# Kernel tuning notes

Hardware: AMD Instinct MI355X
Metric: run time of the kernel (lower is better)

The kernel has to match this reference:

```python
import jax, jax.numpy as jnp
import numpy as np
import math

N_HEAD = 16
HEAD_DIM = 64
N_EMBD = N_HEAD * HEAD_DIM  # 1024


def _alibi_slopes(n_heads):
    def pow2(n):
        start = 2.0 ** (-2.0 ** (-(math.log2(n) - 3)))
        return [start * (start ** i) for i in range(n)]
    if n_heads & (n_heads - 1) == 0:
        s = pow2(n_heads)
    else:
        cp2 = 2 ** math.floor(math.log2(n_heads))
        s = pow2(cp2)
        extra_base = 2.0 ** (-2.0 ** (-(math.log2(2 * cp2) - 3)))
        s += [extra_base * (extra_base ** i) for i in range(n_heads - cp2)]
        s = s[:n_heads]
    return jnp.asarray(np.array(s, dtype=np.float32))


def setup_inputs() -> dict:
    key = jax.random.key(0)
    k1, k2, k3, k4 = jax.random.split(key, 4)
    B, T = 2, 2048
    x = jax.random.normal(k1, (B, T, N_EMBD), dtype=jnp.float32)
    # c_attn weight for q,k (use_v=True -> 2*n_embd outputs), no bias
    W_attn = jax.random.normal(k2, (N_EMBD, 2 * N_EMBD), dtype=jnp.float32) * 0.02
    v_tmp = jax.random.normal(k3, (N_HEAD, N_HEAD), dtype=jnp.float32) * 0.02
    proj_tmp = jax.random.normal(k4, (N_HEAD, N_HEAD), dtype=jnp.float32) * 0.02
    return {"x": x, "W_attn": W_attn, "v_tmp": v_tmp, "proj_tmp": proj_tmp}


def reference(x, W_attn, v_tmp, proj_tmp):
    B, T, C = x.shape
    H, D = N_HEAD, HEAD_DIM
    scale = 1.0 / math.sqrt(D)

    qk = x @ W_attn  # (B,T,2C)
    q, k = qk[..., :C], qk[..., C:]
    q = q.reshape(B, T, H, D).transpose(0, 2, 1, 3)  # (B,H,T,D)
    k = k.reshape(B, T, H, D).transpose(0, 2, 1, 3)

    # V via Kronecker-lifted matrix: x @ kron(v_tmp, I_D)
    # block structure => mix head channels: out[...,j,d] = sum_i x[...,i,d]*v_tmp[i,j]
    xh = x.reshape(B, T, H, D)
    v = jnp.einsum('btid,ij->btjd', xh, v_tmp)  # (B,T,H,D)

    scores = jnp.einsum('bhqd,bhkd->bhqk', q, k) * scale  # (B,H,T,T)

    # ALiBi bias + causal mask
    pos = jnp.arange(T, dtype=jnp.float32)
    rel = pos[None, :] - pos[:, None]  # (T,T), mem - ctx
    slopes = _alibi_slopes(H)
    bias = slopes[:, None, None] * rel[None, :, :]
    causal = pos[None, :] <= pos[:, None]
    bias = jnp.where(causal[None, :, :], bias, -jnp.inf)
    scores = scores + bias[None]

    att = jax.nn.softmax(scores, axis=-1)
    y = jnp.einsum('bhqk,bkhd->bqhd', att, v)  # (B,T,H,D)

    # output proj via kron(proj_tmp, I_D).T: out[...,i,d] = sum_j y[...,j,d]*proj_tmp[i,j]
    y = jnp.einsum('btjd,ij->btid', y, proj_tmp)
    return y.reshape(B, T, C)
```

## Files before the change

kernel.cpp:

```cpp
#include <hip/hip_runtime.h>

typedef __attribute__((ext_vector_type(8))) __bf16 bf16x8;
typedef __attribute__((ext_vector_type(8))) unsigned short u16x8;
typedef __attribute__((ext_vector_type(4))) float f32x4;

#define LOG2E 1.4426950408889634f

__device__ __forceinline__ unsigned short f2b(float f) {
  unsigned u = __float_as_uint(f);
  u += 0x7fffu + ((u >> 16) & 1u);
  return (unsigned short)(u >> 16);
}
__device__ __forceinline__ float b2f(unsigned short h) {
  return __uint_as_float(((unsigned)h) << 16);
}

__global__ __launch_bounds__(256) void k_cvt_x(const float* __restrict__ in,
                                               unsigned short* __restrict__ out, int n4) {
  int i = blockIdx.x * blockDim.x + threadIdx.x;
  if (i >= n4) return;
  float4 f = ((const float4*)in)[i];
  ushort4 o;
  o.x = f2b(f.x); o.y = f2b(f.y); o.z = f2b(f.z); o.w = f2b(f.w);
  ((ushort4*)out)[i] = o;
}

__global__ __launch_bounds__(256) void k_trans_w(const float* __restrict__ W,
                                                 unsigned short* __restrict__ Wt) {
  __shared__ unsigned short tile[64][65];
  int n0 = blockIdx.x * 64;
  int k0 = blockIdx.y * 64;
  int tx = threadIdx.x & 63, ty = threadIdx.x >> 6;
#pragma unroll
  for (int r = 0; r < 16; ++r) {
    int kk = ty * 16 + r;
    tile[kk][tx] = f2b(W[(size_t)(k0 + kk) * 2048 + n0 + tx]);
  }
  __syncthreads();
#pragma unroll
  for (int r = 0; r < 16; ++r) {
    int nn = ty * 16 + r;
    Wt[(size_t)(n0 + nn) * 1024 + k0 + tx] = tile[tx][nn];
  }
}

__global__ __launch_bounds__(256) void k_gemm_qk(const unsigned short* __restrict__ A,
                                                 const unsigned short* __restrict__ Bt,
                                                 unsigned short* __restrict__ C) {
  __shared__ unsigned short As[128 * 32];
  __shared__ unsigned short Bs[128 * 32];
  const int K = 1024;
  int m0 = blockIdx.x * 128;
  int n0 = blockIdx.y * 128;
  int tid = threadIdx.x;
  int w = tid >> 6, lane = tid & 63;
  int lq = lane & 15, lk8 = (lane >> 4) * 8;
  int wr = (w >> 1) * 64, wc = (w & 1) * 64;
  f32x4 acc[4][4];
#pragma unroll
  for (int i = 0; i < 4; ++i)
#pragma unroll
    for (int j = 0; j < 4; ++j)
#pragma unroll
      for (int r = 0; r < 4; ++r) acc[i][j][r] = 0.f;

  for (int kk = 0; kk < K; kk += 32) {
    bf16x8 sa[2], sb[2];
#pragma unroll
    for (int i = 0; i < 2; ++i) {
      int c = tid + 256 * i;
      int row = c >> 2, col = (c & 3) * 8;
      sa[i] = *(const bf16x8*)(A + (size_t)(m0 + row) * K + kk + col);
      sb[i] = *(const bf16x8*)(Bt + (size_t)(n0 + row) * K + kk + col);
    }
    __syncthreads();
#pragma unroll
    for (int i = 0; i < 2; ++i) {
      int c = tid + 256 * i;
      int row = c >> 2, col = (c & 3) * 8;
      *(bf16x8*)(As + row * 32 + col) = sa[i];
      *(bf16x8*)(Bs + row * 32 + col) = sb[i];
    }
    __syncthreads();
    bf16x8 af[4], bf[4];
#pragma unroll
    for (int i = 0; i < 4; ++i) af[i] = *(const bf16x8*)(As + (wr + i * 16 + lq) * 32 + lk8);
#pragma unroll
    for (int j = 0; j < 4; ++j) bf[j] = *(const bf16x8*)(Bs + (wc + j * 16 + lq) * 32 + lk8);
#pragma unroll
    for (int i = 0; i < 4; ++i)
#pragma unroll
      for (int j = 0; j < 4; ++j)
        acc[i][j] = __builtin_amdgcn_mfma_f32_16x16x32_bf16(af[i], bf[j], acc[i][j], 0, 0, 0);
  }
#pragma unroll
  for (int i = 0; i < 4; ++i)
#pragma unroll
    for (int j = 0; j < 4; ++j)
#pragma unroll
      for (int r = 0; r < 4; ++r) {
        int m = m0 + wr + i * 16 + (lane >> 4) * 4 + r;
        int n = n0 + wc + j * 16 + lq;
        C[(size_t)m * 2048 + n] = f2b(acc[i][j][r]);
      }
}

__global__ __launch_bounds__(256) void k_vcomp(const float* __restrict__ x,
                                               const float* __restrict__ vt,
                                               unsigned short* __restrict__ vb) {
  __shared__ float s_vt[256];
  s_vt[threadIdx.x] = vt[threadIdx.x];
  __syncthreads();
  int g = blockIdx.x * 256 + threadIdx.x;
  int bt = g >> 6, d = g & 63;
  const float* xp = x + (size_t)bt * 1024 + d;
  float xi[16];
#pragma unroll
  for (int i = 0; i < 16; ++i) xi[i] = xp[i * 64];
#pragma unroll
  for (int j = 0; j < 16; ++j) {
    float s = 0.f;
#pragma unroll
    for (int i = 0; i < 16; ++i) s += xi[i] * s_vt[i * 16 + j];
    vb[(size_t)bt * 1024 + j * 64 + d] = f2b(s);
  }
}

__global__ __launch_bounds__(256) void k_vtrans(const unsigned short* __restrict__ vb,
                                                unsigned short* __restrict__ Vt) {
  __shared__ unsigned short tile[64][65];
  int t0 = blockIdx.x * 64;
  int c0 = blockIdx.y * 64;
  int b = blockIdx.z;
  int tx = threadIdx.x & 63, ty = threadIdx.x >> 6;
#pragma unroll
  for (int r = 0; r < 16; ++r) {
    int tt = ty * 16 + r;
    tile[tt][tx] = vb[((size_t)b * 2048 + t0 + tt) * 1024 + c0 + tx];
  }
  __syncthreads();
#pragma unroll
  for (int r = 0; r < 16; ++r) {
    int cc = ty * 16 + r;
    Vt[((size_t)b * 1024 + c0 + cc) * 2048 + t0 + tx] = tile[tx][cc];
  }
}

__global__ __launch_bounds__(256) void k_flash(const unsigned short* __restrict__ qkb,
                                               const unsigned short* __restrict__ Vt,
                                               unsigned short* __restrict__ y) {
  __shared__ unsigned short Ks[2][2][64 * 32];
  __shared__ unsigned short Vs[2][2][64 * 32];
  __shared__ unsigned short Pbuf[4][16 * 64];
  int hd = blockIdx.y, b = blockIdx.z;
  int tid = threadIdx.x;
  int w = tid >> 6, lane = tid & 63;
  int quad = lane >> 4, lq = lane & 15, lk8 = quad * 8;
  int rs = tid >> 2, cs = (tid & 3) * 8;
  const size_t rowb = (size_t)b * 2048;
  const size_t vrow = ((size_t)b * 1024 + hd * 64 + rs) * 2048 + cs;
  const size_t krow = ((rowb + rs) << 11) + 1024 + hd * 64 + cs;

  float slope = exp2f(-0.5f * (float)(hd + 1));
  const float c1 = 0.125f * LOG2E;
  const float c2 = slope * LOG2E;
  const float SHIFT = 16.0f;

  bf16x8 ones;
#pragma unroll
  for (int i = 0; i < 8; ++i) ones[i] = (__bf16)1.0f;

#pragma unroll 1
  for (int pass = 0; pass < 2; ++pass) {
    int qt = pass ? (31 - (int)blockIdx.x) : (int)blockIdx.x;
    int q0 = qt * 64;
    int qg = q0 + w * 16 + lq;

    bf16x8 qf0 = *(const bf16x8*)(qkb + ((rowb + qg) << 11) + hd * 64 + lk8);
    bf16x8 qf1 = *(const bf16x8*)(qkb + ((rowb + qg) << 11) + hd * 64 + 32 + lk8);

    int qrow_base = q0 + w * 16 + quad * 4;

    f32x4 o[4], o4;
#pragma unroll
    for (int r = 0; r < 4; ++r) o4[r] = 0.f;
#pragma unroll
    for (int j = 0; j < 4; ++j)
#pragma unroll
      for (int r = 0; r < 4; ++r) o[j][r] = 0.f;

    {
      u16x8 pk0 = *(const u16x8*)(qkb + krow);
      u16x8 pk1 = *(const u16x8*)(qkb + krow + 32);
      u16x8 pv0 = *(const u16x8*)(Vt + vrow);
      u16x8 pv1 = *(const u16x8*)(Vt + vrow + 32);
      __syncthreads();
      *(u16x8*)(&Ks[0][0][rs * 32 + cs]) = pk0;
      *(u16x8*)(&Ks[0][1][rs * 32 + cs]) = pk1;
      *(u16x8*)(&Vs[0][0][rs * 32 + cs]) = pv0;
      *(u16x8*)(&Vs[0][1][rs * 32 + cs]) = pv1;
      __syncthreads();
    }
    int cur = 0;

#pragma unroll 1
    for (int kt = 0; kt <= qt; ++kt) {
      int k0 = kt * 64;
      u16x8 pk0, pk1, pv0, pv1;
      if (kt < qt) {
        size_t koff = (size_t)(k0 + 64);
        pk0 = *(const u16x8*)(qkb + krow + (koff << 11));
        pk1 = *(const u16x8*)(qkb + krow + (koff << 11) + 32);
        pv0 = *(const u16x8*)(Vt + vrow + koff);
        pv1 = *(const u16x8*)(Vt + vrow + koff + 32);
      }
      bf16x8 kc[4][2];
#pragma unroll
      for (int s4 = 0; s4 < 4; ++s4) {
        u16x8 t0 = *(const u16x8*)(&Ks[cur][0][(s4 * 16 + lq) * 32 + lk8]);
        u16x8 t1 = *(const u16x8*)(&Ks[cur][1][(s4 * 16 + lq) * 32 + lk8]);
        kc[s4][0] = __builtin_bit_cast(bf16x8, t0);
        kc[s4][1] = __builtin_bit_cast(bf16x8, t1);
      }
      f32x4 S[4];
#pragma unroll
      for (int s4 = 0; s4 < 4; ++s4) {
        f32x4 a;
#pragma unroll
        for (int r = 0; r < 4; ++r) a[r] = 0.f;
        a = __builtin_amdgcn_mfma_f32_16x16x32_bf16(qf0, kc[s4][0], a, 0, 0, 0);
        a = __builtin_amdgcn_mfma_f32_16x16x32_bf16(qf1, kc[s4][1], a, 0, 0, 0);
        S[s4] = a;
      }
      float p[4][4];
      if (kt == qt) {
#pragma unroll
        for (int s4 = 0; s4 < 4; ++s4) {
          int kg = k0 + s4 * 16 + lq;
#pragma unroll
          for (int r = 0; r < 4; ++r) {
            int qr = qrow_base + r;
            float v = S[s4][r] * c1 + (c2 * (float)(kg - qr) - SHIFT);
            v = (kg <= qr) ? v : -1e30f;
            p[s4][r] = exp2f(v);
          }
        }
      } else {
#pragma unroll
        for (int s4 = 0; s4 < 4; ++s4) {
          int kg = k0 + s4 * 16 + lq;
#pragma unroll
          for (int r = 0; r < 4; ++r) {
            int qr = qrow_base + r;
            float v = S[s4][r] * c1 + (c2 * (float)(kg - qr) - SHIFT);
            p[s4][r] = exp2f(v);
          }
        }
      }
#pragma unroll
      for (int s4 = 0; s4 < 4; ++s4) {
        int cg = (s4 ^ quad) << 4;
#pragma unroll
        for (int r = 0; r < 4; ++r)
          Pbuf[w][(quad * 4 + r) * 64 + cg + lq] = f2b(p[s4][r]);
      }
      int g0 = ((quad >> 1) ^ (lq >> 2)) << 4;
      int g1 = ((2 | (quad >> 1)) ^ (lq >> 2)) << 4;
      int sub = (quad & 1) * 8;
      u16x8 t0 = *(const u16x8*)(&Pbuf[w][lq * 64 + g0 + sub]);
      u16x8 t1 = *(const u16x8*)(&Pbuf[w][lq * 64 + g1 + sub]);
      bf16x8 pf0 = __builtin_bit_cast(bf16x8, t0);
      bf16x8 pf1 = __builtin_bit_cast(bf16x8, t1);
#pragma unroll
      for (int j = 0; j < 4; ++j) {
        u16x8 v0 = *(const u16x8*)(&Vs[cur][0][(j * 16 + lq) * 32 + lk8]);
        u16x8 v1 = *(const u16x8*)(&Vs[cur][1][(j * 16 + lq) * 32 + lk8]);
        bf16x8 vf0 = __builtin_bit_cast(bf16x8, v0);
        bf16x8 vf1 = __builtin_bit_cast(bf16x8, v1);
        o[j] = __builtin_amdgcn_mfma_f32_16x16x32_bf16(pf0, vf0, o[j], 0, 0, 0);
        o[j] = __builtin_amdgcn_mfma_f32_16x16x32_bf16(pf1, vf1, o[j], 0, 0, 0);
        if (j == 0) {
          o4 = __builtin_amdgcn_mfma_f32_16x16x32_bf16(pf0, ones, o4, 0, 0, 0);
          o4 = __builtin_amdgcn_mfma_f32_16x16x32_bf16(pf1, ones, o4, 0, 0, 0);
        }
      }
      if (kt < qt) {
        int nxt = cur ^ 1;
        *(u16x8*)(&Ks[nxt][0][rs * 32 + cs]) = pk0;
        *(u16x8*)(&Ks[nxt][1][rs * 32 + cs]) = pk1;
        *(u16x8*)(&Vs[nxt][0][rs * 32 + cs]) = pv0;
        *(u16x8*)(&Vs[nxt][1][rs * 32 + cs]) = pv1;
        __syncthreads();
        cur = nxt;
      }
    }
#pragma unroll
    for (int r = 0; r < 4; ++r) {
      float inv = 1.0f / o4[r];
      int qr = qrow_base + r;
#pragma unroll
      for (int j = 0; j < 4; ++j)
        y[((rowb + qr) << 10) + hd * 64 + j * 16 + lq] = f2b(o[j][r] * inv);
    }
  }
}

__global__ __launch_bounds__(256) void k_proj(const unsigned short* __restrict__ yb,
                                              const float* __restrict__ pt,
                                              float* __restrict__ out) {
  __shared__ float s_pt[256];
  s_pt[threadIdx.x] = pt[threadIdx.x];
  __syncthreads();
  int g = blockIdx.x * 256 + threadIdx.x;
  int bt = g >> 6, d = g & 63;
  float yj[16];
#pragma unroll
  for (int j = 0; j < 16; ++j) yj[j] = b2f(yb[(size_t)bt * 1024 + j * 64 + d]);
#pragma unroll
  for (int i = 0; i < 16; ++i) {
    float s = 0.f;
#pragma unroll
    for (int j = 0; j < 16; ++j) s += yj[j] * s_pt[i * 16 + j];
    out[(size_t)bt * 1024 + i * 64 + d] = s;
  }
}

extern "C" void kernel_launch(void* const* d_in, const int* in_sizes, int n_in,
                              void* d_out, int out_size, void* d_ws, size_t ws_size,
                              hipStream_t stream) {
  const float* x  = (const float*)d_in[0];
  const float* W  = (const float*)d_in[1];
  const float* vt = (const float*)d_in[2];
  const float* pt = (const float*)d_in[3];
  float* out = (float*)d_out;

  char* ws = (char*)d_ws;
  unsigned short* xb  = (unsigned short*)(ws);
  unsigned short* Wt  = (unsigned short*)(ws + (8u  << 20));
  unsigned short* qkb = (unsigned short*)(ws + (12u << 20));
  unsigned short* vb  = (unsigned short*)(ws + (28u << 20));
  unsigned short* Vtr = (unsigned short*)(ws + (36u << 20));
  unsigned short* yb  = xb;

  k_cvt_x  <<<4096, 256, 0, stream>>>(x, xb, 4194304 / 4);
  k_trans_w<<<dim3(32, 16), 256, 0, stream>>>(W, Wt);
  k_gemm_qk<<<dim3(32, 16), 256, 0, stream>>>(xb, Wt, qkb);
  k_vcomp  <<<1024, 256, 0, stream>>>(x, vt, vb);
  k_vtrans <<<dim3(32, 16, 2), 256, 0, stream>>>(vb, Vtr);
  k_flash  <<<dim3(16, 16, 2), 256, 0, stream>>>(qkb, Vtr, yb);
  k_proj   <<<1024, 256, 0, stream>>>(yb, pt, out);
}
```

Measured before the change: 176.7 us.

## One query tile per flash block with XOR-swizzled K/V shared memory

The flash kernel drops its two-pass pairing, where one block handled query tile i and then tile 31-i. It now launches 32x16x2 blocks, each handling a single query tile, and flips the tile order on alternating head groups to spread the causal load. K and V tiles in shared memory now use an XOR swizzle on the 8-element column chunk, meant to reduce LDS bank conflicts on the fragment reads. The grid doubles to expose more parallelism, but per-block work becomes uneven, so load balance now depends on the hardware scheduler.

```diff
diff --git a/kernel.cpp b/kernel.cpp
--- a/kernel.cpp
+++ b/kernel.cpp
@@ -156,10 +156,12 @@
   int tid = threadIdx.x;
   int w = tid >> 6, lane = tid & 63;
   int quad = lane >> 4, lq = lane & 15, lk8 = quad * 8;
-  int rs = tid >> 2, cs = (tid & 3) * 8;
+  int rs = tid >> 2;
+  int scc = (((tid & 3) ^ ((rs >> 1) & 3)) * 8);
+  int rcc = ((quad ^ ((lq >> 1) & 3)) * 8);
   const size_t rowb = (size_t)b * 2048;
-  const size_t vrow = ((size_t)b * 1024 + hd * 64 + rs) * 2048 + cs;
-  const size_t krow = ((rowb + rs) << 11) + 1024 + hd * 64 + cs;
+  const size_t vrow = ((size_t)b * 1024 + hd * 64 + rs) * 2048 + (tid & 3) * 8;
+  const size_t krow = ((rowb + rs) << 11) + 1024 + hd * 64 + (tid & 3) * 8;
 
   float slope = exp2f(-0.5f * (float)(hd + 1));
   const float c1 = 0.125f * LOG2E;
@@ -170,138 +172,134 @@
 #pragma unroll
   for (int i = 0; i < 8; ++i) ones[i] = (__bf16)1.0f;
 
+  int qt = ((hd >> 2) & 1) ? (31 - (int)blockIdx.x) : (int)blockIdx.x;
+  int q0 = qt * 64;
+  int qg = q0 + w * 16 + lq;
+
+  bf16x8 qf0 = *(const bf16x8*)(qkb + ((rowb + qg) << 11) + hd * 64 + lk8);
+  bf16x8 qf1 = *(const bf16x8*)(qkb + ((rowb + qg) << 11) + hd * 64 + 32 + lk8);
+
+  int qrow_base = q0 + w * 16 + quad * 4;
+
+  f32x4 o[4], o4;
+#pragma unroll
+  for (int r = 0; r < 4; ++r) o4[r] = 0.f;
+#pragma unroll
+  for (int j = 0; j < 4; ++j)
+#pragma unroll
+    for (int r = 0; r < 4; ++r) o[j][r] = 0.f;
+
+  {
+    u16x8 pk0 = *(const u16x8*)(qkb + krow);
+    u16x8 pk1 = *(const u16x8*)(qkb + krow + 32);
+    u16x8 pv0 = *(const u16x8*)(Vt + vrow);
+    u16x8 pv1 = *(const u16x8*)(Vt + vrow + 32);
+    *(u16x8*)(&Ks[0][0][rs * 32 + scc]) = pk0;
+    *(u16x8*)(&Ks[0][1][rs * 32 + scc]) = pk1;
+    *(u16x8*)(&Vs[0][0][rs * 32 + scc]) = pv0;
+    *(u16x8*)(&Vs[0][1][rs * 32 + scc]) = pv1;
+    __syncthreads();
+  }
+  int cur = 0;
+
 #pragma unroll 1
-  for (int pass = 0; pass < 2; ++pass) {
-    int qt = pass ? (31 - (int)blockIdx.x) : (int)blockIdx.x;
-    int q0 = qt * 64;
-    int qg = q0 + w * 16 + lq;
-
-    bf16x8 qf0 = *(const bf16x8*)(qkb + ((rowb + qg) << 11) + hd * 64 + lk8);
-    bf16x8 qf1 = *(const bf16x8*)(qkb + ((rowb + qg) << 11) + hd * 64 + 32 + lk8);
-
-    int qrow_base = q0 + w * 16 + quad * 4;
-
-    f32x4 o[4], o4;
-#pragma unroll
-    for (int r = 0; r < 4; ++r) o4[r] = 0.f;
-#pragma unroll
-    for (int j = 0; j < 4; ++j)
-#pragma unroll
-      for (int r = 0; r < 4; ++r) o[j][r] = 0.f;
-
-    {
-      u16x8 pk0 = *(const u16x8*)(qkb + krow);
-      u16x8 pk1 = *(const u16x8*)(qkb + krow + 32);
-      u16x8 pv0 = *(const u16x8*)(Vt + vrow);
-      u16x8 pv1 = *(const u16x8*)(Vt + vrow + 32);
-      __syncthreads();
-      *(u16x8*)(&Ks[0][0][rs * 32 + cs]) = pk0;
-      *(u16x8*)(&Ks[0][1][rs * 32 + cs]) = pk1;
-      *(u16x8*)(&Vs[0][0][rs * 32 + cs]) = pv0;
-      *(u16x8*)(&Vs[0][1][rs * 32 + cs]) = pv1;
-      __syncthreads();
-    }
-    int cur = 0;
-
-#pragma unroll 1
-    for (int kt = 0; kt <= qt; ++kt) {
-      int k0 = kt * 64;
-      u16x8 pk0, pk1, pv0, pv1;
-      if (kt < qt) {
-        size_t koff = (size_t)(k0 + 64);
-        pk0 = *(const u16x8*)(qkb + krow + (koff << 11));
-        pk1 = *(const u16x8*)(qkb + krow + (koff << 11) + 32);
-        pv0 = *(const u16x8*)(Vt + vrow + koff);
-        pv1 = *(const u16x8*)(Vt + vrow + koff + 32);
-      }
-      bf16x8 kc[4][2];
+  for (int kt = 0; kt <= qt; ++kt) {
+    int k0 = kt * 64;
+    u16x8 pk0, pk1, pv0, pv1;
+    if (kt < qt) {
+      size_t koff = (size_t)(k0 + 64);
+      pk0 = *(const u16x8*)(qkb + krow + (koff << 11));
+      pk1 = *(const u16x8*)(qkb + krow + (koff << 11) + 32);
+      pv0 = *(const u16x8*)(Vt + vrow + koff);
+      pv1 = *(const u16x8*)(Vt + vrow + koff + 32);
+    }
+    bf16x8 kc[4][2];
+#pragma unroll
+    for (int s4 = 0; s4 < 4; ++s4) {
+      u16x8 t0 = *(const u16x8*)(&Ks[cur][0][(s4 * 16 + lq) * 32 + rcc]);
+      u16x8 t1 = *(const u16x8*)(&Ks[cur][1][(s4 * 16 + lq) * 32 + rcc]);
+      kc[s4][0] = __builtin_bit_cast(bf16x8, t0);
+      kc[s4][1] = __builtin_bit_cast(bf16x8, t1);
+    }
+    f32x4 S[4];
+#pragma unroll
+    for (int s4 = 0; s4 < 4; ++s4) {
+      f32x4 a;
+#pragma unroll
+      for (int r = 0; r < 4; ++r) a[r] = 0.f;
+      a = __builtin_amdgcn_mfma_f32_16x16x32_bf16(qf0, kc[s4][0], a, 0, 0, 0);
+      a = __builtin_amdgcn_mfma_f32_16x16x32_bf16(qf1, kc[s4][1], a, 0, 0, 0);
+      S[s4] = a;
+    }
+    float p[4][4];
+    if (kt == qt) {
 #pragma unroll
       for (int s4 = 0; s4 < 4; ++s4) {
-        u16x8 t0 = *(const u16x8*)(&Ks[cur][0][(s4 * 16 + lq) * 32 + lk8]);
-        u16x8 t1 = *(const u16x8*)(&Ks[cur][1][(s4 * 16 + lq) * 32 + lk8]);
-        kc[s4][0] = __builtin_bit_cast(bf16x8, t0);
-        kc[s4][1] = __builtin_bit_cast(bf16x8, t1);
-      }
-      f32x4 S[4];
-#pragma unroll
-      for (int s4 = 0; s4 < 4; ++s4) {
-        f32x4 a;
-#pragma unroll
-        for (int r = 0; r < 4; ++r) a[r] = 0.f;
-        a = __builtin_amdgcn_mfma_f32_16x16x32_bf16(qf0, kc[s4][0], a, 0, 0, 0);
-        a = __builtin_amdgcn_mfma_f32_16x16x32_bf16(qf1, kc[s4][1], a, 0, 0, 0);
-        S[s4] = a;
-      }
-      float p[4][4];
-      if (kt == qt) {
-#pragma unroll
-        for (int s4 = 0; s4 < 4; ++s4) {
-          int kg = k0 + s4 * 16 + lq;
-#pragma unroll
-          for (int r = 0; r < 4; ++r) {
-            int qr = qrow_base + r;
-            float v = S[s4][r] * c1 + (c2 * (float)(kg - qr) - SHIFT);
-            v = (kg <= qr) ? v : -1e30f;
-            p[s4][r] = exp2f(v);
-          }
-        }
-      } else {
-#pragma unroll
-        for (int s4 = 0; s4 < 4; ++s4) {
-          int kg = k0 + s4 * 16 + lq;
-#pragma unroll
-          for (int r = 0; r < 4; ++r) {
-            int qr = qrow_base + r;
-            float v = S[s4][r] * c1 + (c2 * (float)(kg - qr) - SHIFT);
-            p[s4][r] = exp2f(v);
-          }
+        int kg = k0 + s4 * 16 + lq;
+#pragma unroll
+        for (int r = 0; r < 4; ++r) {
+          int qr = qrow_base + r;
+          float v = S[s4][r] * c1 + (c2 * (float)(kg - qr) - SHIFT);
+          v = (kg <= qr) ? v : -1e30f;
+          p[s4][r] = exp2f(v);
         }
       }
+    } else {
 #pragma unroll
       for (int s4 = 0; s4 < 4; ++s4) {
-        int cg = (s4 ^ quad) << 4;
-#pragma unroll
-        for (int r = 0; r < 4; ++r)
-          Pbuf[w][(quad * 4 + r) * 64 + cg + lq] = f2b(p[s4][r]);
-      }
-      int g0 = ((quad >> 1) ^ (lq >> 2)) << 4;
-      int g1 = ((2 | (quad >> 1)) ^ (lq >> 2)) << 4;
-      int sub = (quad & 1) * 8;
-      u16x8 t0 = *(const u16x8*)(&Pbuf[w][lq * 64 + g0 + sub]);
-      u16x8 t1 = *(const u16x8*)(&Pbuf[w][lq * 64 + g1 + sub]);
-      bf16x8 pf0 = __builtin_bit_cast(bf16x8, t0);
-      bf16x8 pf1 = __builtin_bit_cast(bf16x8, t1);
-#pragma unroll
-      for (int j = 0; j < 4; ++j) {
-        u16x8 v0 = *(const u16x8*)(&Vs[cur][0][(j * 16 + lq) * 32 + lk8]);
-        u16x8 v1 = *(const u16x8*)(&Vs[cur][1][(j * 16 + lq) * 32 + lk8]);
-        bf16x8 vf0 = __builtin_bit_cast(bf16x8, v0);
-        bf16x8 vf1 = __builtin_bit_cast(bf16x8, v1);
-        o[j] = __builtin_amdgcn_mfma_f32_16x16x32_bf16(pf0, vf0, o[j], 0, 0, 0);
-        o[j] = __builtin_amdgcn_mfma_f32_16x16x32_bf16(pf1, vf1, o[j], 0, 0, 0);
-        if (j == 0) {
-          o4 = __builtin_amdgcn_mfma_f32_16x16x32_bf16(pf0, ones, o4, 0, 0, 0);
-          o4 = __builtin_amdgcn_mfma_f32_16x16x32_bf16(pf1, ones, o4, 0, 0, 0);
+        int kg = k0 + s4 * 16 + lq;
+#pragma unroll
+        for (int r = 0; r < 4; ++r) {
+          int qr = qrow_base + r;
+          float v = S[s4][r] * c1 + (c2 * (float)(kg - qr) - SHIFT);
+          p[s4][r] = exp2f(v);
         }
       }
-      if (kt < qt) {
-        int nxt = cur ^ 1;
-        *(u16x8*)(&Ks[nxt][0][rs * 32 + cs]) = pk0;
-        *(u16x8*)(&Ks[nxt][1][rs * 32 + cs]) = pk1;
-        *(u16x8*)(&Vs[nxt][0][rs * 32 + cs]) = pv0;
-        *(u16x8*)(&Vs[nxt][1][rs * 32 + cs]) = pv1;
-        __syncthreads();
-        cur = nxt;
+    }
+#pragma unroll
+    for (int s4 = 0; s4 < 4; ++s4) {
+      int cg = (s4 ^ quad) << 4;
+#pragma unroll
+      for (int r = 0; r < 4; ++r)
+        Pbuf[w][(quad * 4 + r) * 64 + cg + lq] = f2b(p[s4][r]);
+    }
+    int g0 = ((quad >> 1) ^ (lq >> 2)) << 4;
+    int g1 = ((2 | (quad >> 1)) ^ (lq >> 2)) << 4;
+    int sub = (quad & 1) * 8;
+    u16x8 t0 = *(const u16x8*)(&Pbuf[w][lq * 64 + g0 + sub]);
+    u16x8 t1 = *(const u16x8*)(&Pbuf[w][lq * 64 + g1 + sub]);
+    bf16x8 pf0 = __builtin_bit_cast(bf16x8, t0);
+    bf16x8 pf1 = __builtin_bit_cast(bf16x8, t1);
+#pragma unroll
+    for (int j = 0; j < 4; ++j) {
+      u16x8 v0 = *(const u16x8*)(&Vs[cur][0][(j * 16 + lq) * 32 + rcc]);
+      u16x8 v1 = *(const u16x8*)(&Vs[cur][1][(j * 16 + lq) * 32 + rcc]);
+      bf16x8 vf0 = __builtin_bit_cast(bf16x8, v0);
+      bf16x8 vf1 = __builtin_bit_cast(bf16x8, v1);
+      o[j] = __builtin_amdgcn_mfma_f32_16x16x32_bf16(pf0, vf0, o[j], 0, 0, 0);
+      o[j] = __builtin_amdgcn_mfma_f32_16x16x32_bf16(pf1, vf1, o[j], 0, 0, 0);
+      if (j == 0) {
+        o4 = __builtin_amdgcn_mfma_f32_16x16x32_bf16(pf0, ones, o4, 0, 0, 0);
+        o4 = __builtin_amdgcn_mfma_f32_16x16x32_bf16(pf1, ones, o4, 0, 0, 0);
       }
     }
-#pragma unroll
-    for (int r = 0; r < 4; ++r) {
-      float inv = 1.0f / o4[r];
-      int qr = qrow_base + r;
-#pragma unroll
-      for (int j = 0; j < 4; ++j)
-        y[((rowb + qr) << 10) + hd * 64 + j * 16 + lq] = f2b(o[j][r] * inv);
-    }
+    if (kt < qt) {
+      int nxt = cur ^ 1;
+      *(u16x8*)(&Ks[nxt][0][rs * 32 + scc]) = pk0;
+      *(u16x8*)(&Ks[nxt][1][rs * 32 + scc]) = pk1;
+      *(u16x8*)(&Vs[nxt][0][rs * 32 + scc]) = pv0;
+      *(u16x8*)(&Vs[nxt][1][rs * 32 + scc]) = pv1;
+      __syncthreads();
+      cur = nxt;
+    }
+  }
+#pragma unroll
+  for (int r = 0; r < 4; ++r) {
+    float inv = 1.0f / o4[r];
+    int qr = qrow_base + r;
+#pragma unroll
+    for (int j = 0; j < 4; ++j)
+      y[((rowb + qr) << 10) + hd * 64 + j * 16 + lq] = f2b(o[j][r] * inv);
   }
 }
 
@@ -347,6 +345,6 @@
   k_gemm_qk<<<dim3(32, 16), 256, 0, stream>>>(xb, Wt, qkb);
   k_vcomp  <<<1024, 256, 0, stream>>>(x, vt, vb);
   k_vtrans <<<dim3(32, 16, 2), 256, 0, stream>>>(vb, Vtr);
-  k_flash  <<<dim3(16, 16, 2), 256, 0, stream>>>(qkb, Vtr, yb);
+  k_flash  <<<dim3(32, 16, 2), 256, 0, stream>>>(qkb, Vtr, yb);
   k_proj   <<<1024, 256, 0, stream>>>(yb, pt, out);
 }
```

New measurement: 189.7 us. +7.3%, slower.
